# Optimization experiments

Hardware: AMD Instinct MI355X
Metric: run time of the kernel (lower is better)

The kernel has to match this reference:

```python
import jax, jax.numpy as jnp
import numpy as np

B, N, H = 4, 256, 128
T = 8  # triplet hidden width


def _linear_init(key, fan_in, fan_out):
    s = 1.0 / np.sqrt(fan_in)
    kw, kb = jax.random.split(key)
    W = jax.random.uniform(kw, (fan_in, fan_out), minval=-s, maxval=s, dtype=jnp.float32)
    b = jax.random.uniform(kb, (fan_out,), minval=-s, maxval=s, dtype=jnp.float32)
    return W, b


def setup_inputs() -> dict:
    key = jax.random.key(0)
    ks = jax.random.split(key, 16)
    inp = {
        "node_embeddings": jax.random.normal(ks[0], (B, N, H), dtype=jnp.float32),
        "edge_embeddings": jax.random.normal(ks[1], (B, N, H), dtype=jnp.float32),
        "graph_embeddings": jax.random.normal(ks[2], (B, H), dtype=jnp.float32),
        "previous_hidden": jax.random.normal(ks[3], (B, N, H), dtype=jnp.float32),
    }
    # message MLP: (z_i 2H, z_j 2H, edge_j H, graph H) = 6H -> H -> H -> H
    inp["Wm1"], inp["bm1"] = _linear_init(ks[4], 6 * H, H)
    inp["Wm2"], inp["bm2"] = _linear_init(ks[5], H, H)
    inp["Wm3"], inp["bm3"] = _linear_init(ks[6], H, H)
    # gate MLP: (z 2H, m H, edge H, graph H) = 5H -> H -> H (sigmoid)
    inp["Wg1"], inp["bg1"] = _linear_init(ks[7], 5 * H, H)
    inp["Wg2"], inp["bg2"] = _linear_init(ks[8], H, H)
    # readout: (z 2H, m H) = 3H -> H
    inp["Wr"], inp["br"] = _linear_init(ks[9], 3 * H, H)
    # triplet MLP: (node_j H, node_k H, node H, edge 3H, graph H) = 7H -> 8 (relu)
    inp["Wt1"], inp["bt1"] = _linear_init(ks[10], 7 * H, T)
    # triplet edge readout: 8 -> H
    inp["Wt2"], inp["bt2"] = _linear_init(ks[11], T, H)
    # layer norm params
    inp["gamma"] = jnp.ones((H,), dtype=jnp.float32)
    inp["beta"] = jnp.zeros((H,), dtype=jnp.float32)
    return inp


def reference(node_embeddings, edge_embeddings, graph_embeddings, previous_hidden,
              Wm1, bm1, Wm2, bm2, Wm3, bm3,
              Wg1, bg1, Wg2, bg2, Wr, br,
              Wt1, bt1, Wt2, bt2, gamma, beta):
    h = node_embeddings.shape[-1]
    z = jnp.concatenate([node_embeddings, previous_hidden], axis=-1)  # [B,N,2H]

    # ---- pairwise messages: decompose first linear so the 6H-wide concat is never built ----
    W_zi, W_zj = Wm1[: 2 * h], Wm1[2 * h: 4 * h]
    W_e, W_g = Wm1[4 * h: 5 * h], Wm1[5 * h:]
    u = z @ W_zi + (graph_embeddings @ W_g)[:, None, :] + bm1   # per-i part [B,N,H]
    v = z @ W_zj + edge_embeddings @ W_e                        # per-j part [B,N,H]
    h1 = jax.nn.relu(u[:, :, None, :] + v[:, None, :, :])       # [B,Ni,Nj,H]
    h2 = jax.nn.relu(h1 @ Wm2 + bm2)
    msgs = h2 @ Wm3 + bm3                                       # [B,Ni,Nj,H]
    m = jnp.max(msgs, axis=2)                                   # max over j -> [B,N,H]

    gb = jnp.broadcast_to(graph_embeddings[:, None, :], node_embeddings.shape)
    gate_in = jnp.concatenate([z, m, edge_embeddings, gb], axis=-1)  # [B,N,5H]
    g = jax.nn.sigmoid(jax.nn.relu(gate_in @ Wg1 + bg1) @ Wg2 + bg2)
    h_i = jnp.concatenate([z, m], axis=-1) @ Wr + br
    h_g = g * h_i + (1.0 - g) * previous_hidden

    # ---- triplet messages ----
    # pre-activation is separable over (j, k, i), so max over the N^2 (k,j) pairs
    # equals per-channel max_j + max_k (relu is monotone, max commutes with it).
    Wt_j, Wt_k, Wt_n = Wt1[:h], Wt1[h: 2 * h], Wt1[2 * h: 3 * h]
    Wt_e = Wt1[3 * h: 4 * h] + Wt1[4 * h: 5 * h] + Wt1[5 * h: 6 * h]
    Wt_g = Wt1[6 * h:]
    a_j = node_embeddings @ Wt_j   # [B,N,8]
    a_k = node_embeddings @ Wt_k   # [B,N,8]
    c = node_embeddings @ Wt_n + edge_embeddings @ Wt_e + (graph_embeddings @ Wt_g)[:, None, :] + bt1
    t_max = jax.nn.relu(c + jnp.max(a_j, axis=1, keepdims=True) + jnp.max(a_k, axis=1, keepdims=True))
    h_ij = t_max @ Wt2 + bt2       # [B,N,H]

    # ---- layer norm on gated hidden ----
    mu = jnp.mean(h_g, axis=-1, keepdims=True)
    var = jnp.mean(jnp.square(h_g - mu), axis=-1, keepdims=True)
    h_norm = (h_g - mu) * jax.lax.rsqrt(var + 1e-5) * gamma + beta
    return (h_norm, h_ij)
```

## Files before the change

### kernel.cpp

```cpp
#include <hip/hip_runtime.h>
#include <hip/hip_bf16.h>

typedef unsigned short u16;
typedef unsigned int u32;
typedef float f32x4 __attribute__((ext_vector_type(4)));
typedef float f32x16 __attribute__((ext_vector_type(16)));
typedef short s16x8 __attribute__((ext_vector_type(8)));

#define MFMA32(a,b,c) __builtin_amdgcn_mfma_f32_32x32x16_bf16((a),(b),(c),0,0,0)
#define MFMA16(a,b,c) __builtin_amdgcn_mfma_f32_16x16x32_bf16((a),(b),(c),0,0,0)

static __device__ __forceinline__ u16 f2bf(float x){
  union { __hip_bfloat16 b; u16 u; } c;
  c.b = __float2bfloat16(x);
  return c.u;
}
static __device__ __forceinline__ u32 pk2(float a, float b){
  return (u32)f2bf(a) | ((u32)f2bf(b) << 16);
}

static __device__ __forceinline__ void softbar() {
  __builtin_amdgcn_sched_barrier(0);
  asm volatile("s_waitcnt lgkmcnt(0)" ::: "memory");
  __builtin_amdgcn_s_barrier();
  __builtin_amdgcn_sched_barrier(0);
}

__global__ void prep_kernel(const float* __restrict__ Wm1, const float* __restrict__ Wm2,
                            const float* __restrict__ Wm3, const float* __restrict__ Wg1,
                            const float* __restrict__ Wr,  const float* __restrict__ Wt1,
                            const float* __restrict__ node,const float* __restrict__ prev,
                            const float* __restrict__ edge,const float* __restrict__ graph,
                            u16* __restrict__ WbT, u16* __restrict__ WgrT,
                            u16* __restrict__ Wm2T, u16* __restrict__ Wm3T,
                            u16* __restrict__ gin)
{
  int idx = blockIdx.x * 256 + threadIdx.x;
  if (idx < 147456) {
    int n = idx >> 9, k = idx & 511;
    int part = k >> 7, kk = k & 127;
    float v = 0.f;
    if (n < 128) {
      if (part == 0)      v = Wm1[kk*128 + n];
      else if (part == 1) v = Wm1[(128+kk)*128 + n];
      else if (part == 3) v = Wm1[(640+kk)*128 + n];
    } else if (n < 256) {
      int nn = n - 128;
      if (part == 0)      v = Wm1[(256+kk)*128 + nn];
      else if (part == 1) v = Wm1[(384+kk)*128 + nn];
      else if (part == 2) v = Wm1[(512+kk)*128 + nn];
    } else if (n < 280) {
      int tt = n - 256;
      if (tt < 8)       { if (part == 0) v = Wt1[kk*8 + tt]; }
      else if (tt < 16) { if (part == 0) v = Wt1[(128+kk)*8 + (tt-8)]; }
      else {
        int t = tt - 16;
        if (part == 0)      v = Wt1[(256+kk)*8 + t];
        else if (part == 2) v = Wt1[(384+kk)*8 + t] + Wt1[(512+kk)*8 + t] + Wt1[(640+kk)*8 + t];
        else if (part == 3) v = Wt1[(768+kk)*8 + t];
      }
    }
    WbT[idx] = f2bf(v);
    return;
  }
  idx -= 147456;
  if (idx < 163840) {
    int n = idx / 640, k = idx - n*640;
    int part = k >> 7, kk = k & 127;
    float v = 0.f;
    if (n < 128) {
      int r = (part==0) ? kk : (part==1) ? (128+kk) : (part==2) ? (384+kk)
                        : (part==3) ? (512+kk) : (256+kk);
      v = Wg1[r*128 + n];
    } else {
      int nn = n - 128;
      if (part == 0)      v = Wr[kk*128 + nn];
      else if (part == 1) v = Wr[(128+kk)*128 + nn];
      else if (part == 4) v = Wr[(256+kk)*128 + nn];
    }
    WgrT[idx] = f2bf(v);
    return;
  }
  idx -= 163840;
  if (idx < 16384) { int n = idx >> 7, k = idx & 127; Wm2T[idx] = f2bf(Wm2[k*128 + n]); return; }
  idx -= 16384;
  if (idx < 16384) { int n = idx >> 7, k = idx & 127; Wm3T[idx] = f2bf(Wm3[k*128 + n]); return; }
  idx -= 16384;
  {
    int row = idx >> 9, k = idx & 511;
    int part = k >> 7, kk = k & 127;
    float v;
    if (part == 0)      v = node[row*128 + kk];
    else if (part == 1) v = prev[row*128 + kk];
    else if (part == 2) v = edge[row*128 + kk];
    else                v = graph[(row >> 8)*128 + kk];
    gin[row*640 + k] = f2bf(v);
  }
}

__global__ __launch_bounds__(256) void gemm_uvt_kernel(const u16* __restrict__ gin,
                                                       const u16* __restrict__ WbT,
                                                       float* __restrict__ uvt)
{
  int m0 = blockIdx.x * 16, n0 = blockIdx.y * 16;
  int tid = threadIdx.x;
  int w = tid >> 6, lane = tid & 63;
  int c = lane & 15, g = lane >> 4;
  __shared__ float cpart[4][16][17];
  const u16* arow = gin + (size_t)(m0 + c) * 640;
  const u16* brow = WbT + (size_t)(n0 + c) * 512;
  f32x4 acc = {0.f, 0.f, 0.f, 0.f};
#pragma unroll
  for (int kk = 0; kk < 4; ++kk) {
    int k0 = w*4 + kk;
    s16x8 a = *reinterpret_cast<const s16x8*>(arow + k0*32 + g*8);
    s16x8 b = *reinterpret_cast<const s16x8*>(brow + k0*32 + g*8);
    acc = MFMA16(a, b, acc);
  }
#pragma unroll
  for (int r = 0; r < 4; ++r) cpart[w][g*4 + r][c] = acc[r];
  __syncthreads();
  int row = tid >> 4, col = tid & 15;
  float s = cpart[0][row][col] + cpart[1][row][col]
          + cpart[2][row][col] + cpart[3][row][col];
  uvt[(size_t)(m0 + row) * 288 + n0 + col] = s;
}

__global__ __launch_bounds__(256) void msgmax_kernel(const float* __restrict__ uvt,
    const u16* __restrict__ Wm2T, const u16* __restrict__ Wm3T,
    const float* __restrict__ bm1, const float* __restrict__ bm2,
    const float* __restrict__ bm3, u16* __restrict__ gin, float* __restrict__ mjk)
{
  const int row = blockIdx.x;
  const int b   = row >> 8;
  const int tid = threadIdx.x;
  const int w   = tid >> 6;
  const int lane = tid & 63;
  const int jc = lane & 31;
  const int hi = lane >> 5;
  const int colbase = w * 32;

  __shared__ u16 a1s[32][136];
  __shared__ u16 h2s[32][136];
  __shared__ float part[4][16];

  s16x8 wb2[8], wb3[8];
#pragma unroll
  for (int ks = 0; ks < 8; ++ks) {
    wb2[ks] = *reinterpret_cast<const s16x8*>(Wm2T + (colbase + jc)*128 + ks*16 + hi*8);
    wb3[ks] = *reinterpret_cast<const s16x8*>(Wm3T + (colbase + jc)*128 + ks*16 + hi*8);
  }

  const int bj = lane >> 3;
  const int bk = (lane & 7) * 16;
  f32x4 uf[4];
  {
    const float* urow = uvt + (size_t)row * 288;
#pragma unroll
    for (int q = 0; q < 4; ++q)
      uf[q] = *reinterpret_cast<const f32x4*>(urow + bk + q*4)
            + *reinterpret_cast<const f32x4*>(bm1 + bk + q*4);
  }
  f32x4 bm2v[4];
#pragma unroll
  for (int grp = 0; grp < 4; ++grp)
    bm2v[grp] = *reinterpret_cast<const f32x4*>(bm2 + colbase + grp*8 + 4*hi);

  const f32x4 z4 = {0.f, 0.f, 0.f, 0.f};
  float mm[16];
#pragma unroll
  for (int i = 0; i < 16; ++i) mm[i] = -1e30f;

  const float* vb = uvt + (size_t)(b*256) * 288 + 128;
  f32x4 vc[4];
#define LOADV(IT) do { \
  const float* p_ = vb + (size_t)((IT)*32 + w*8 + bj) * 288 + bk; \
  vc[0] = *reinterpret_cast<const f32x4*>(p_); \
  vc[1] = *reinterpret_cast<const f32x4*>(p_ + 4); \
  vc[2] = *reinterpret_cast<const f32x4*>(p_ + 8); \
  vc[3] = *reinterpret_cast<const f32x4*>(p_ + 12); } while (0)

  LOADV(0);

  for (int it = 0; it < 8; ++it) {
#pragma unroll
    for (int q = 0; q < 2; ++q) {
      f32x4 lo = __builtin_elementwise_max(vc[2*q]   + uf[2*q],   z4);
      f32x4 hn = __builtin_elementwise_max(vc[2*q+1] + uf[2*q+1], z4);
      uint4 pk = {pk2(lo[0], lo[1]), pk2(lo[2], lo[3]),
                  pk2(hn[0], hn[1]), pk2(hn[2], hn[3])};
      *reinterpret_cast<uint4*>(&a1s[w*8 + bj][bk + q*8]) = pk;
    }
    if (it < 7) LOADV(it + 1);
    softbar();

    f32x16 acc1;
#pragma unroll
    for (int grp = 0; grp < 4; ++grp)
#pragma unroll
      for (int r = 0; r < 4; ++r) acc1[grp*4 + r] = bm2v[grp][r];
#pragma unroll
    for (int ks = 0; ks < 8; ++ks) {
      s16x8 bf = *reinterpret_cast<const s16x8*>(&a1s[jc][ks*16 + hi*8]);
      acc1 = MFMA32(wb2[ks], bf, acc1);
    }
#pragma unroll
    for (int grp = 0; grp < 4; ++grp) {
      float v0 = fmaxf(acc1[grp*4+0], 0.f), v1 = fmaxf(acc1[grp*4+1], 0.f);
      float v2 = fmaxf(acc1[grp*4+2], 0.f), v3 = fmaxf(acc1[grp*4+3], 0.f);
      uint2 pk = {pk2(v0, v1), pk2(v2, v3)};
      *reinterpret_cast<uint2*>(&h2s[jc][colbase + grp*8 + 4*hi]) = pk;
    }
    softbar();

    f32x16 acc2 = {0.f,0.f,0.f,0.f,0.f,0.f,0.f,0.f,
                   0.f,0.f,0.f,0.f,0.f,0.f,0.f,0.f};
#pragma unroll
    for (int ks = 0; ks < 8; ++ks) {
      s16x8 bf = *reinterpret_cast<const s16x8*>(&h2s[jc][ks*16 + hi*8]);
      acc2 = MFMA32(wb3[ks], bf, acc2);
    }
#pragma unroll
    for (int i = 0; i < 16; ++i) mm[i] = fmaxf(mm[i], acc2[i]);
  }
#undef LOADV

#pragma unroll
  for (int i = 0; i < 16; ++i) {
    mm[i] = fmaxf(mm[i], __shfl_xor(mm[i], 1));
    mm[i] = fmaxf(mm[i], __shfl_xor(mm[i], 2));
    mm[i] = fmaxf(mm[i], __shfl_xor(mm[i], 4));
    mm[i] = fmaxf(mm[i], __shfl_xor(mm[i], 8));
    mm[i] = fmaxf(mm[i], __shfl_xor(mm[i], 16));
  }
  if (jc == 0) {
#pragma unroll
    for (int grp = 0; grp < 4; ++grp) {
      int col = colbase + grp*8 + 4*hi;
      uint2 pk = {pk2(mm[grp*4+0] + bm3[col],   mm[grp*4+1] + bm3[col+1]),
                  pk2(mm[grp*4+2] + bm3[col+2], mm[grp*4+3] + bm3[col+3])};
      *reinterpret_cast<uint2*>(gin + (size_t)row*640 + 512 + col) = pk;
    }
  }

  if (row < 4) {
    __syncthreads();
    int rr = row*256 + tid;
    float v[16];
#pragma unroll
    for (int t = 0; t < 16; ++t) v[t] = uvt[(size_t)rr*288 + 256 + t];
#pragma unroll
    for (int off = 32; off >= 1; off >>= 1) {
#pragma unroll
      for (int t = 0; t < 16; ++t) v[t] = fmaxf(v[t], __shfl_xor(v[t], off));
    }
    int wid = tid >> 6;
    if ((tid & 63) == 0) {
#pragma unroll
      for (int t = 0; t < 16; ++t) part[wid][t] = v[t];
    }
    __syncthreads();
    if (tid < 16)
      mjk[row*16 + tid] = fmaxf(fmaxf(part[0][tid], part[1][tid]),
                                fmaxf(part[2][tid], part[3][tid]));
  }
}

__global__ __launch_bounds__(256) void gemm_gate_kernel(const u16* __restrict__ gin,
                                 const u16* __restrict__ WgrT,
                                 const float* __restrict__ bg1, const float* __restrict__ br,
                                 float* __restrict__ r1, float* __restrict__ hi)
{
  int m0 = blockIdx.x * 16, n0 = blockIdx.y * 16;
  int tid = threadIdx.x;
  int w = tid >> 6, lane = tid & 63;
  int c = lane & 15, g = lane >> 4;
  __shared__ float cpart[4][16][17];
  const u16* arow = gin  + (size_t)(m0 + c) * 640;
  const u16* brow = WgrT + (size_t)(n0 + c) * 640;
  f32x4 acc = {0.f, 0.f, 0.f, 0.f};
#pragma unroll
  for (int kk = 0; kk < 5; ++kk) {
    int k0 = w*5 + kk;
    s16x8 a = *reinterpret_cast<const s16x8*>(arow + k0*32 + g*8);
    s16x8 b = *reinterpret_cast<const s16x8*>(brow + k0*32 + g*8);
    acc = MFMA16(a, b, acc);
  }
#pragma unroll
  for (int r = 0; r < 4; ++r) cpart[w][g*4 + r][c] = acc[r];
  __syncthreads();
  int row = tid >> 4, col = tid & 15;
  float s = cpart[0][row][col] + cpart[1][row][col]
          + cpart[2][row][col] + cpart[3][row][col];
  int coln = n0 + col;
  int gr = m0 + row;
  if (coln < 128) r1[gr*128 + coln] = fmaxf(s + bg1[coln], 0.f);
  else            hi[gr*128 + coln - 128] = s + br[coln - 128];
}

__global__ void finalize_kernel(const float* __restrict__ r1, const float* __restrict__ hi,
                                const float* __restrict__ prev, const float* __restrict__ uvt,
                                const float* __restrict__ mjk,
                                const float* __restrict__ Wg2, const float* __restrict__ bg2,
                                const float* __restrict__ bt1, const float* __restrict__ Wt2,
                                const float* __restrict__ bt2, const float* __restrict__ gamma,
                                const float* __restrict__ beta, float* __restrict__ out)
{
  int row = blockIdx.x;
  int h = threadIdx.x;
  int b = row >> 8;
  __shared__ float r1s[128];
  __shared__ float red[4];
  r1s[h] = r1[row*128 + h];
  __syncthreads();
  float glin = bg2[h];
#pragma unroll 8
  for (int k = 0; k < 128; ++k) glin += r1s[k] * Wg2[k*128 + h];
  float g = 1.f / (1.f + __expf(-glin));
  float hg = g * hi[row*128 + h] + (1.f - g) * prev[row*128 + h];

  float s1 = hg, s2 = hg*hg;
#pragma unroll
  for (int off = 1; off < 64; off <<= 1) {
    s1 += __shfl_xor(s1, off);
    s2 += __shfl_xor(s2, off);
  }
  int wid = h >> 6;
  if ((h & 63) == 0) { red[wid] = s1; red[2 + wid] = s2; }
  __syncthreads();
  float mu  = (red[0] + red[1]) * 0.0078125f;
  float ex2 = (red[2] + red[3]) * 0.0078125f;
  float var = ex2 - mu*mu;
  float hn = (hg - mu) * rsqrtf(var + 1e-5f) * gamma[h] + beta[h];
  out[row*128 + h] = hn;

  float o2 = bt2[h];
#pragma unroll
  for (int t = 0; t < 8; ++t) {
    float tv = uvt[(size_t)row*288 + 272 + t] + bt1[t] + mjk[b*16 + t] + mjk[b*16 + 8 + t];
    tv = fmaxf(tv, 0.f);
    o2 += tv * Wt2[t*128 + h];
  }
  out[131072 + row*128 + h] = o2;
}

extern "C" void kernel_launch(void* const* d_in, const int* in_sizes, int n_in,
                              void* d_out, int out_size, void* d_ws, size_t ws_size,
                              hipStream_t stream) {
  const float* node  = (const float*)d_in[0];
  const float* edge  = (const float*)d_in[1];
  const float* graph = (const float*)d_in[2];
  const float* prev  = (const float*)d_in[3];
  const float* Wm1 = (const float*)d_in[4];
  const float* bm1 = (const float*)d_in[5];
  const float* Wm2 = (const float*)d_in[6];
  const float* bm2 = (const float*)d_in[7];
  const float* Wm3 = (const float*)d_in[8];
  const float* bm3 = (const float*)d_in[9];
  const float* Wg1 = (const float*)d_in[10];
  const float* bg1 = (const float*)d_in[11];
  const float* Wg2 = (const float*)d_in[12];
  const float* bg2 = (const float*)d_in[13];
  const float* Wr  = (const float*)d_in[14];
  const float* br  = (const float*)d_in[15];
  const float* Wt1 = (const float*)d_in[16];
  const float* bt1 = (const float*)d_in[17];
  const float* Wt2 = (const float*)d_in[18];
  const float* bt2 = (const float*)d_in[19];
  const float* gamma = (const float*)d_in[20];
  const float* beta  = (const float*)d_in[21];
  float* out = (float*)d_out;

  char* ws = (char*)d_ws;
  u16*   WbT  = (u16*)(ws + 0);
  u16*   WgrT = (u16*)(ws + 294912);
  u16*   Wm2T = (u16*)(ws + 622592);
  u16*   Wm3T = (u16*)(ws + 655360);
  u16*   gin  = (u16*)(ws + 688128);
  float* uvt  = (float*)(ws + 1998848);
  float* r1   = (float*)(ws + 3178496);
  float* hi   = (float*)(ws + 3702784);
  float* mjk  = (float*)(ws + 4227072);

  prep_kernel<<<3392, 256, 0, stream>>>(Wm1, Wm2, Wm3, Wg1, Wr, Wt1,
                                        node, prev, edge, graph,
                                        WbT, WgrT, Wm2T, Wm3T, gin);
  gemm_uvt_kernel<<<dim3(64, 18), 256, 0, stream>>>(gin, WbT, uvt);
  msgmax_kernel<<<1024, 256, 0, stream>>>(uvt, Wm2T, Wm3T, bm1, bm2, bm3, gin, mjk);
  gemm_gate_kernel<<<dim3(64, 16), 256, 0, stream>>>(gin, WgrT, bg1, br, r1, hi);
  finalize_kernel<<<1024, 128, 0, stream>>>(r1, hi, prev, uvt, mjk,
                                            Wg2, bg2, bt1, Wt2, bt2, gamma, beta, out);
}
```

Measured before the change: 62.08 us.

## Fuse gate GEMM with finalize and process two rows per msgmax block

Merges the gate/readout GEMM and the finalize kernel into one kernel that keeps r1 and the readout in shared memory and runs the Wg2 product on MFMA with a bf16-transposed Wg2 prepared in the prep kernel. msgmax now handles two query rows per block, so each loaded v tile and the register-resident weights are reused twice and half as many blocks are launched. This removes one launch and the r1/hi round trips through global memory. In exchange the fused kernel runs only 64 blocks, which leaves much of the GPU idle, and the Wg2 product is now computed in bf16.

```diff
diff --git a/kernel.cpp b/kernel.cpp
--- a/kernel.cpp
+++ b/kernel.cpp
@@ -29,11 +29,12 @@
 __global__ void prep_kernel(const float* __restrict__ Wm1, const float* __restrict__ Wm2,
                             const float* __restrict__ Wm3, const float* __restrict__ Wg1,
                             const float* __restrict__ Wr,  const float* __restrict__ Wt1,
+                            const float* __restrict__ Wg2,
                             const float* __restrict__ node,const float* __restrict__ prev,
                             const float* __restrict__ edge,const float* __restrict__ graph,
                             u16* __restrict__ WbT, u16* __restrict__ WgrT,
                             u16* __restrict__ Wm2T, u16* __restrict__ Wm3T,
-                            u16* __restrict__ gin)
+                            u16* __restrict__ Wg2T, u16* __restrict__ gin)
 {
   int idx = blockIdx.x * 256 + threadIdx.x;
   if (idx < 147456) {
@@ -86,6 +87,8 @@
   idx -= 16384;
   if (idx < 16384) { int n = idx >> 7, k = idx & 127; Wm3T[idx] = f2bf(Wm3[k*128 + n]); return; }
   idx -= 16384;
+  if (idx < 16384) { int n = idx >> 7, k = idx & 127; Wg2T[idx] = f2bf(Wg2[k*128 + n]); return; }
+  idx -= 16384;
   {
     int row = idx >> 9, k = idx & 511;
     int part = k >> 7, kk = k & 127;
@@ -131,8 +134,9 @@
     const float* __restrict__ bm1, const float* __restrict__ bm2,
     const float* __restrict__ bm3, u16* __restrict__ gin, float* __restrict__ mjk)
 {
-  const int row = blockIdx.x;
-  const int b   = row >> 8;
+  const int bx   = blockIdx.x;
+  const int row0 = bx * 2;
+  const int b    = row0 >> 8;
   const int tid = threadIdx.x;
   const int w   = tid >> 6;
   const int lane = tid & 63;
@@ -140,8 +144,8 @@
   const int hi = lane >> 5;
   const int colbase = w * 32;
 
-  __shared__ u16 a1s[32][136];
-  __shared__ u16 h2s[32][136];
+  __shared__ u16 a1s[2][32][136];
+  __shared__ u16 h2s[2][32][136];
   __shared__ float part[4][16];
 
   s16x8 wb2[8], wb3[8];
@@ -153,13 +157,14 @@
 
   const int bj = lane >> 3;
   const int bk = (lane & 7) * 16;
-  f32x4 uf[4];
-  {
-    const float* urow = uvt + (size_t)row * 288;
+  f32x4 uf[2][4];
+#pragma unroll
+  for (int i = 0; i < 2; ++i) {
+    const float* urow = uvt + (size_t)(row0 + i) * 288;
 #pragma unroll
     for (int q = 0; q < 4; ++q)
-      uf[q] = *reinterpret_cast<const f32x4*>(urow + bk + q*4)
-            + *reinterpret_cast<const f32x4*>(bm1 + bk + q*4);
+      uf[i][q] = *reinterpret_cast<const f32x4*>(urow + bk + q*4)
+               + *reinterpret_cast<const f32x4*>(bm1 + bk + q*4);
   }
   f32x4 bm2v[4];
 #pragma unroll
@@ -167,9 +172,11 @@
     bm2v[grp] = *reinterpret_cast<const f32x4*>(bm2 + colbase + grp*8 + 4*hi);
 
   const f32x4 z4 = {0.f, 0.f, 0.f, 0.f};
-  float mm[16];
-#pragma unroll
-  for (int i = 0; i < 16; ++i) mm[i] = -1e30f;
+  float mm[2][16];
+#pragma unroll
+  for (int i = 0; i < 2; ++i)
+#pragma unroll
+    for (int t = 0; t < 16; ++t) mm[i][t] = -1e30f;
 
   const float* vb = uvt + (size_t)(b*256) * 288 + 128;
   f32x4 vc[4];
@@ -184,68 +191,80 @@
 
   for (int it = 0; it < 8; ++it) {
 #pragma unroll
-    for (int q = 0; q < 2; ++q) {
-      f32x4 lo = __builtin_elementwise_max(vc[2*q]   + uf[2*q],   z4);
-      f32x4 hn = __builtin_elementwise_max(vc[2*q+1] + uf[2*q+1], z4);
-      uint4 pk = {pk2(lo[0], lo[1]), pk2(lo[2], lo[3]),
-                  pk2(hn[0], hn[1]), pk2(hn[2], hn[3])};
-      *reinterpret_cast<uint4*>(&a1s[w*8 + bj][bk + q*8]) = pk;
+    for (int i = 0; i < 2; ++i) {
+#pragma unroll
+      for (int q = 0; q < 2; ++q) {
+        f32x4 lo = __builtin_elementwise_max(vc[2*q]   + uf[i][2*q],   z4);
+        f32x4 hn = __builtin_elementwise_max(vc[2*q+1] + uf[i][2*q+1], z4);
+        uint4 pk = {pk2(lo[0], lo[1]), pk2(lo[2], lo[3]),
+                    pk2(hn[0], hn[1]), pk2(hn[2], hn[3])};
+        *reinterpret_cast<uint4*>(&a1s[i][w*8 + bj][bk + q*8]) = pk;
+      }
     }
     if (it < 7) LOADV(it + 1);
     softbar();
 
-    f32x16 acc1;
-#pragma unroll
-    for (int grp = 0; grp < 4; ++grp)
-#pragma unroll
-      for (int r = 0; r < 4; ++r) acc1[grp*4 + r] = bm2v[grp][r];
-#pragma unroll
-    for (int ks = 0; ks < 8; ++ks) {
-      s16x8 bf = *reinterpret_cast<const s16x8*>(&a1s[jc][ks*16 + hi*8]);
-      acc1 = MFMA32(wb2[ks], bf, acc1);
-    }
-#pragma unroll
-    for (int grp = 0; grp < 4; ++grp) {
-      float v0 = fmaxf(acc1[grp*4+0], 0.f), v1 = fmaxf(acc1[grp*4+1], 0.f);
-      float v2 = fmaxf(acc1[grp*4+2], 0.f), v3 = fmaxf(acc1[grp*4+3], 0.f);
-      uint2 pk = {pk2(v0, v1), pk2(v2, v3)};
-      *reinterpret_cast<uint2*>(&h2s[jc][colbase + grp*8 + 4*hi]) = pk;
+#pragma unroll
+    for (int i = 0; i < 2; ++i) {
+      f32x16 acc1;
+#pragma unroll
+      for (int grp = 0; grp < 4; ++grp)
+#pragma unroll
+        for (int r = 0; r < 4; ++r) acc1[grp*4 + r] = bm2v[grp][r];
+#pragma unroll
+      for (int ks = 0; ks < 8; ++ks) {
+        s16x8 bf = *reinterpret_cast<const s16x8*>(&a1s[i][jc][ks*16 + hi*8]);
+        acc1 = MFMA32(wb2[ks], bf, acc1);
+      }
+#pragma unroll
+      for (int grp = 0; grp < 4; ++grp) {
+        float v0 = fmaxf(acc1[grp*4+0], 0.f), v1 = fmaxf(acc1[grp*4+1], 0.f);
+        float v2 = fmaxf(acc1[grp*4+2], 0.f), v3 = fmaxf(acc1[grp*4+3], 0.f);
+        uint2 pk = {pk2(v0, v1), pk2(v2, v3)};
+        *reinterpret_cast<uint2*>(&h2s[i][jc][colbase + grp*8 + 4*hi]) = pk;
+      }
     }
     softbar();
 
-    f32x16 acc2 = {0.f,0.f,0.f,0.f,0.f,0.f,0.f,0.f,
-                   0.f,0.f,0.f,0.f,0.f,0.f,0.f,0.f};
-#pragma unroll
-    for (int ks = 0; ks < 8; ++ks) {
-      s16x8 bf = *reinterpret_cast<const s16x8*>(&h2s[jc][ks*16 + hi*8]);
-      acc2 = MFMA32(wb3[ks], bf, acc2);
-    }
-#pragma unroll
-    for (int i = 0; i < 16; ++i) mm[i] = fmaxf(mm[i], acc2[i]);
+#pragma unroll
+    for (int i = 0; i < 2; ++i) {
+      f32x16 acc2 = {0.f,0.f,0.f,0.f,0.f,0.f,0.f,0.f,
+                     0.f,0.f,0.f,0.f,0.f,0.f,0.f,0.f};
+#pragma unroll
+      for (int ks = 0; ks < 8; ++ks) {
+        s16x8 bf = *reinterpret_cast<const s16x8*>(&h2s[i][jc][ks*16 + hi*8]);
+        acc2 = MFMA32(wb3[ks], bf, acc2);
+      }
+#pragma unroll
+      for (int t = 0; t < 16; ++t) mm[i][t] = fmaxf(mm[i][t], acc2[t]);
+    }
   }
 #undef LOADV
 
 #pragma unroll
-  for (int i = 0; i < 16; ++i) {
-    mm[i] = fmaxf(mm[i], __shfl_xor(mm[i], 1));
-    mm[i] = fmaxf(mm[i], __shfl_xor(mm[i], 2));
-    mm[i] = fmaxf(mm[i], __shfl_xor(mm[i], 4));
-    mm[i] = fmaxf(mm[i], __shfl_xor(mm[i], 8));
-    mm[i] = fmaxf(mm[i], __shfl_xor(mm[i], 16));
-  }
-  if (jc == 0) {
-#pragma unroll
-    for (int grp = 0; grp < 4; ++grp) {
-      int col = colbase + grp*8 + 4*hi;
-      uint2 pk = {pk2(mm[grp*4+0] + bm3[col],   mm[grp*4+1] + bm3[col+1]),
-                  pk2(mm[grp*4+2] + bm3[col+2], mm[grp*4+3] + bm3[col+3])};
-      *reinterpret_cast<uint2*>(gin + (size_t)row*640 + 512 + col) = pk;
-    }
-  }
-
-  if (row < 4) {
+  for (int i = 0; i < 2; ++i) {
+#pragma unroll
+    for (int t = 0; t < 16; ++t) {
+      mm[i][t] = fmaxf(mm[i][t], __shfl_xor(mm[i][t], 1));
+      mm[i][t] = fmaxf(mm[i][t], __shfl_xor(mm[i][t], 2));
+      mm[i][t] = fmaxf(mm[i][t], __shfl_xor(mm[i][t], 4));
+      mm[i][t] = fmaxf(mm[i][t], __shfl_xor(mm[i][t], 8));
+      mm[i][t] = fmaxf(mm[i][t], __shfl_xor(mm[i][t], 16));
+    }
+    if (jc == 0) {
+#pragma unroll
+      for (int grp = 0; grp < 4; ++grp) {
+        int col = colbase + grp*8 + 4*hi;
+        uint2 pk = {pk2(mm[i][grp*4+0] + bm3[col],   mm[i][grp*4+1] + bm3[col+1]),
+                    pk2(mm[i][grp*4+2] + bm3[col+2], mm[i][grp*4+3] + bm3[col+3])};
+        *reinterpret_cast<uint2*>(gin + (size_t)(row0 + i)*640 + 512 + col) = pk;
+      }
+    }
+  }
+
+  if (bx < 4) {
     __syncthreads();
-    int rr = row*256 + tid;
+    int rr = bx*256 + tid;
     float v[16];
 #pragma unroll
     for (int t = 0; t < 16; ++t) v[t] = uvt[(size_t)rr*288 + 256 + t];
@@ -261,87 +280,125 @@
     }
     __syncthreads();
     if (tid < 16)
-      mjk[row*16 + tid] = fmaxf(fmaxf(part[0][tid], part[1][tid]),
-                                fmaxf(part[2][tid], part[3][tid]));
-  }
-}
-
-__global__ __launch_bounds__(256) void gemm_gate_kernel(const u16* __restrict__ gin,
-                                 const u16* __restrict__ WgrT,
-                                 const float* __restrict__ bg1, const float* __restrict__ br,
-                                 float* __restrict__ r1, float* __restrict__ hi)
+      mjk[bx*16 + tid] = fmaxf(fmaxf(part[0][tid], part[1][tid]),
+                               fmaxf(part[2][tid], part[3][tid]));
+  }
+}
+
+__global__ __launch_bounds__(256) void gate_finalize_kernel(
+    const u16* __restrict__ gin, const u16* __restrict__ WgrT,
+    const u16* __restrict__ Wg2T,
+    const float* __restrict__ bg1, const float* __restrict__ br,
+    const float* __restrict__ bg2, const float* __restrict__ prev,
+    const float* __restrict__ uvt, const float* __restrict__ mjk,
+    const float* __restrict__ bt1, const float* __restrict__ Wt2,
+    const float* __restrict__ bt2, const float* __restrict__ gamma,
+    const float* __restrict__ beta, float* __restrict__ out)
 {
-  int m0 = blockIdx.x * 16, n0 = blockIdx.y * 16;
-  int tid = threadIdx.x;
-  int w = tid >> 6, lane = tid & 63;
-  int c = lane & 15, g = lane >> 4;
-  __shared__ float cpart[4][16][17];
-  const u16* arow = gin  + (size_t)(m0 + c) * 640;
-  const u16* brow = WgrT + (size_t)(n0 + c) * 640;
-  f32x4 acc = {0.f, 0.f, 0.f, 0.f};
-#pragma unroll
-  for (int kk = 0; kk < 5; ++kk) {
-    int k0 = w*5 + kk;
-    s16x8 a = *reinterpret_cast<const s16x8*>(arow + k0*32 + g*8);
-    s16x8 b = *reinterpret_cast<const s16x8*>(brow + k0*32 + g*8);
-    acc = MFMA16(a, b, acc);
-  }
-#pragma unroll
-  for (int r = 0; r < 4; ++r) cpart[w][g*4 + r][c] = acc[r];
+  const int m0 = blockIdx.x * 16;
+  const int tid = threadIdx.x;
+  const int w = tid >> 6, lane = tid & 63;
+  const int c = lane & 15, g = lane >> 4;
+
+  __shared__ u16 at[16][648];
+  __shared__ u16 r1b[16][136];
+  __shared__ float his[16][132];
+  __shared__ float gls[16][132];
+
+#pragma unroll
+  for (int q = 0; q < 5; ++q) {
+    int idx = q*256 + tid;
+    int r = idx / 80, kk = (idx - r*80) * 8;
+    *reinterpret_cast<uint4*>(&at[r][kk]) =
+      *reinterpret_cast<const uint4*>(gin + (size_t)(m0 + r)*640 + kk);
+  }
   __syncthreads();
-  int row = tid >> 4, col = tid & 15;
-  float s = cpart[0][row][col] + cpart[1][row][col]
-          + cpart[2][row][col] + cpart[3][row][col];
-  int coln = n0 + col;
-  int gr = m0 + row;
-  if (coln < 128) r1[gr*128 + coln] = fmaxf(s + bg1[coln], 0.f);
-  else            hi[gr*128 + coln - 128] = s + br[coln - 128];
-}
-
-__global__ void finalize_kernel(const float* __restrict__ r1, const float* __restrict__ hi,
-                                const float* __restrict__ prev, const float* __restrict__ uvt,
-                                const float* __restrict__ mjk,
-                                const float* __restrict__ Wg2, const float* __restrict__ bg2,
-                                const float* __restrict__ bt1, const float* __restrict__ Wt2,
-                                const float* __restrict__ bt2, const float* __restrict__ gamma,
-                                const float* __restrict__ beta, float* __restrict__ out)
-{
-  int row = blockIdx.x;
-  int h = threadIdx.x;
-  int b = row >> 8;
-  __shared__ float r1s[128];
-  __shared__ float red[4];
-  r1s[h] = r1[row*128 + h];
+
+#pragma unroll
+  for (int nt = 0; nt < 4; ++nt) {
+    int n0 = w*64 + nt*16;
+    const u16* brow = WgrT + (size_t)(n0 + c) * 640;
+    f32x4 acc = {0.f, 0.f, 0.f, 0.f};
+#pragma unroll
+    for (int k0 = 0; k0 < 20; ++k0) {
+      s16x8 a = *reinterpret_cast<const s16x8*>(&at[c][k0*32 + g*8]);
+      s16x8 b = *reinterpret_cast<const s16x8*>(brow + k0*32 + g*8);
+      acc = MFMA16(a, b, acc);
+    }
+    int ocol = n0 + c;
+#pragma unroll
+    for (int r = 0; r < 4; ++r) {
+      int orow = g*4 + r;
+      if (ocol < 128) {
+        float val = fmaxf(acc[r] + bg1[ocol], 0.f);
+        r1b[orow][ocol] = f2bf(val);
+      } else {
+        his[orow][ocol - 128] = acc[r] + br[ocol - 128];
+      }
+    }
+  }
   __syncthreads();
-  float glin = bg2[h];
-#pragma unroll 8
-  for (int k = 0; k < 128; ++k) glin += r1s[k] * Wg2[k*128 + h];
-  float g = 1.f / (1.f + __expf(-glin));
-  float hg = g * hi[row*128 + h] + (1.f - g) * prev[row*128 + h];
-
-  float s1 = hg, s2 = hg*hg;
-#pragma unroll
-  for (int off = 1; off < 64; off <<= 1) {
+
+#pragma unroll
+  for (int nt = 0; nt < 2; ++nt) {
+    int n0 = w*32 + nt*16;
+    const u16* brow = Wg2T + (size_t)(n0 + c) * 128;
+    f32x4 acc = {0.f, 0.f, 0.f, 0.f};
+#pragma unroll
+    for (int k0 = 0; k0 < 4; ++k0) {
+      s16x8 a = *reinterpret_cast<const s16x8*>(&r1b[c][k0*32 + g*8]);
+      s16x8 b = *reinterpret_cast<const s16x8*>(brow + k0*32 + g*8);
+      acc = MFMA16(a, b, acc);
+    }
+    int ocol = n0 + c;
+#pragma unroll
+    for (int r = 0; r < 4; ++r)
+      gls[g*4 + r][ocol] = acc[r] + bg2[ocol];
+  }
+  __syncthreads();
+
+  const int row = tid >> 4;
+  const int cb = (tid & 15) * 8;
+  const int grow = m0 + row;
+  const int bb = grow >> 8;
+  const float* prow = prev + (size_t)grow * 128 + cb;
+
+  float hgv[8];
+  float s1 = 0.f, s2 = 0.f;
+#pragma unroll
+  for (int q = 0; q < 8; ++q) {
+    float gl = gls[row][cb + q];
+    float gg = 1.f / (1.f + __expf(-gl));
+    float hg = gg * his[row][cb + q] + (1.f - gg) * prow[q];
+    hgv[q] = hg; s1 += hg; s2 += hg*hg;
+  }
+#pragma unroll
+  for (int off = 1; off < 16; off <<= 1) {
     s1 += __shfl_xor(s1, off);
     s2 += __shfl_xor(s2, off);
   }
-  int wid = h >> 6;
-  if ((h & 63) == 0) { red[wid] = s1; red[2 + wid] = s2; }
-  __syncthreads();
-  float mu  = (red[0] + red[1]) * 0.0078125f;
-  float ex2 = (red[2] + red[3]) * 0.0078125f;
-  float var = ex2 - mu*mu;
-  float hn = (hg - mu) * rsqrtf(var + 1e-5f) * gamma[h] + beta[h];
-  out[row*128 + h] = hn;
-
-  float o2 = bt2[h];
-#pragma unroll
-  for (int t = 0; t < 8; ++t) {
-    float tv = uvt[(size_t)row*288 + 272 + t] + bt1[t] + mjk[b*16 + t] + mjk[b*16 + 8 + t];
-    tv = fmaxf(tv, 0.f);
-    o2 += tv * Wt2[t*128 + h];
-  }
-  out[131072 + row*128 + h] = o2;
+  float mu  = s1 * 0.0078125f;
+  float var = s2 * 0.0078125f - mu*mu;
+  float rs  = rsqrtf(var + 1e-5f);
+#pragma unroll
+  for (int q = 0; q < 8; ++q) {
+    int col = cb + q;
+    out[(size_t)grow*128 + col] = (hgv[q] - mu) * rs * gamma[col] + beta[col];
+  }
+
+  float tv[8];
+  const float* crow = uvt + (size_t)grow * 288 + 272;
+#pragma unroll
+  for (int t = 0; t < 8; ++t)
+    tv[t] = fmaxf(crow[t] + bt1[t] + mjk[bb*16 + t] + mjk[bb*16 + 8 + t], 0.f);
+#pragma unroll
+  for (int q = 0; q < 8; ++q) {
+    int col = cb + q;
+    float o2 = bt2[col];
+#pragma unroll
+    for (int t = 0; t < 8; ++t) o2 += tv[t] * Wt2[t*128 + col];
+    out[131072 + (size_t)grow*128 + col] = o2;
+  }
 }
 
 extern "C" void kernel_launch(void* const* d_in, const int* in_sizes, int n_in,
@@ -378,16 +435,15 @@
   u16*   Wm3T = (u16*)(ws + 655360);
   u16*   gin  = (u16*)(ws + 688128);
   float* uvt  = (float*)(ws + 1998848);
-  float* r1   = (float*)(ws + 3178496);
-  float* hi   = (float*)(ws + 3702784);
-  float* mjk  = (float*)(ws + 4227072);
-
-  prep_kernel<<<3392, 256, 0, stream>>>(Wm1, Wm2, Wm3, Wg1, Wr, Wt1,
+  u16*   Wg2T = (u16*)(ws + 3178496);
+  float* mjk  = (float*)(ws + 3211264);
+
+  prep_kernel<<<3456, 256, 0, stream>>>(Wm1, Wm2, Wm3, Wg1, Wr, Wt1, Wg2,
                                         node, prev, edge, graph,
-                                        WbT, WgrT, Wm2T, Wm3T, gin);
+                                        WbT, WgrT, Wm2T, Wm3T, Wg2T, gin);
   gemm_uvt_kernel<<<dim3(64, 18), 256, 0, stream>>>(gin, WbT, uvt);
-  msgmax_kernel<<<1024, 256, 0, stream>>>(uvt, Wm2T, Wm3T, bm1, bm2, bm3, gin, mjk);
-  gemm_gate_kernel<<<dim3(64, 16), 256, 0, stream>>>(gin, WgrT, bg1, br, r1, hi);
-  finalize_kernel<<<1024, 128, 0, stream>>>(r1, hi, prev, uvt, mjk,
-                                            Wg2, bg2, bt1, Wt2, bt2, gamma, beta, out);
-}
+  msgmax_kernel<<<512, 256, 0, stream>>>(uvt, Wm2T, Wm3T, bm1, bm2, bm3, gin, mjk);
+  gate_finalize_kernel<<<64, 256, 0, stream>>>(gin, WgrT, Wg2T, bg1, br, bg2,
+                                               prev, uvt, mjk, bt1, Wt2, bt2,
+                                               gamma, beta, out);
+}
```

Result: slower. 64.20 us (+3.4%).
